# Optimization experiments

Measured on AMD Instinct MI355X. Metric: run time of the kernel, lower is better.

## Reference

```python
import jax, jax.numpy as jnp
import numpy as np

NNZ = 3355443          # int(4096*4096*(1-0.8))
IN_FEATURES = 4096
OUT_FEATURES = 4096
BATCH = 64
ACTIVE_THRESHOLD = 0.01


def setup_inputs() -> dict:
    key = jax.random.key(0)
    k1, k2, k3, k4 = jax.random.split(key, 4)
    x = jax.random.uniform(k1, (BATCH, IN_FEATURES), dtype=jnp.float32)
    row_indices = jax.random.randint(k2, (NNZ,), 0, OUT_FEATURES, dtype=jnp.int32)
    col_indices = jax.random.randint(k3, (NNZ,), 0, IN_FEATURES, dtype=jnp.int32)
    values = jax.random.normal(k4, (NNZ,), dtype=jnp.float32)
    bias = jnp.zeros((OUT_FEATURES,), dtype=jnp.float32)
    return {"x": x, "row_indices": row_indices, "col_indices": col_indices,
            "values": values, "bias": bias}


def reference(x, row_indices, col_indices, values, bias):
    # Event-driven gating: only columns with x > threshold contribute.
    # Equivalent to masking x, then a standard COO spmv per batch row.
    xm = jnp.where(x > ACTIVE_THRESHOLD, x, jnp.zeros((), x.dtype))   # [B, in]
    contrib = values[None, :] * xm[:, col_indices]                    # [B, nnz]
    out = jnp.zeros((x.shape[0], bias.shape[0]), dtype=x.dtype)
    out = out.at[:, row_indices].add(contrib)                         # scatter-add over rows
    return out + bias[None, :]
```

## Files before the change

kernel.cpp:

```cpp
#include <hip/hip_runtime.h>
#include <hip/hip_bf16.h>
#include <stdint.h>

#define IN_F 4096
#define OUT_F 4096
#define NBIN 512
#define SBLOCKS 410
#define REC_PER_SB 8192
#define SMAX 7424u
#define THRESH 0.01f

typedef unsigned int u32;
typedef unsigned short u16;
typedef __attribute__((ext_vector_type(8))) short short8;
typedef __attribute__((ext_vector_type(4))) float f32x4;

static constexpr size_t pad256(size_t x) { return (x + 255u) & ~(size_t)255u; }
static constexpr size_t WS_XB   = 0;
static constexpr size_t WS_CUR  = pad256(WS_XB + (size_t)512 * 64 * 8 * 2);
static constexpr size_t WS_BINS = pad256(WS_CUR + (size_t)NBIN * 4);
static constexpr size_t WS_PART = pad256(WS_BINS + (size_t)NBIN * SMAX * 4);
static constexpr size_t WS_NEEDED = WS_PART + (size_t)NBIN * 4096 * 4;

static __device__ __forceinline__ u16 f2bf(float v) {
  __hip_bfloat16 h = __float2bfloat16(v);
  return *reinterpret_cast<u16*>(&h);
}

__global__ __launch_bounds__(512) void k_init(u32* __restrict__ cur) {
  cur[threadIdx.x] = 0u;
}

__global__ __launch_bounds__(1024) void k_scatter(const int* __restrict__ rows,
                                                  const int* __restrict__ cols,
                                                  const float* __restrict__ vals, u32 nnz,
                                                  const float* __restrict__ x,
                                                  u16* __restrict__ xB,
                                                  u32* __restrict__ gcursor,
                                                  u32* __restrict__ sortb) {
  __shared__ u32 cnt[NBIN];
  __shared__ u32 pref[NBIN + 1];
  __shared__ u32 gbase[NBIN];
  __shared__ u32 srt[REC_PER_SB];
  __shared__ u16 srtb[REC_PER_SB];
  const int tid = threadIdx.x;
  const int lane = tid & 63;
  const int wid = tid >> 6;

  if (blockIdx.x < 32) {
    const int g = blockIdx.x * 1024 + tid;
    const int b = g & 63;
    const int kg = g >> 6;
    const float* src = x + (size_t)b * IN_F + kg * 8;
    const f32x4 a0 = *reinterpret_cast<const f32x4*>(src);
    const f32x4 a1 = *reinterpret_cast<const f32x4*>(src + 4);
    short8 o;
#pragma unroll
    for (int e = 0; e < 4; ++e) { float v = a0[e]; o[e] = (short)f2bf(v > THRESH ? v : 0.f); }
#pragma unroll
    for (int e = 0; e < 4; ++e) { float v = a1[e]; o[4 + e] = (short)f2bf(v > THRESH ? v : 0.f); }
    *reinterpret_cast<short8*>(xB + ((size_t)kg * 64 + b) * 8) = o;
  }

  if (tid < NBIN) cnt[tid] = 0;
  __syncthreads();
  const u32 base_i = blockIdx.x * (u32)REC_PER_SB;
  u32 rec[8], bkt[8], rk[8];
#pragma unroll
  for (int j = 0; j < 8; ++j) {
    const u32 i = base_i + (u32)j * 1024u + tid;
    bkt[j] = 0xffffffffu;
    if (i < nnz) {
      const u32 r = (u32)rows[i] & 4095u;
      const u32 c = (u32)cols[i] & 4095u;
      rec[j] = ((c & 511u) << 22) | ((r & 63u) << 16) | (u32)f2bf(vals[i]);
      bkt[j] = ((r >> 6) << 3) | (c >> 9);
      rk[j] = atomicAdd(&cnt[bkt[j]], 1u);
    }
  }
  __syncthreads();
  if (wid == 0) {
    u32 a[8]; u32 s = 0;
#pragma unroll
    for (int j = 0; j < 8; ++j) { a[j] = cnt[lane * 8 + j]; s += a[j]; }
    u32 xx = s;
#pragma unroll
    for (int d = 1; d < 64; d <<= 1) {
      const u32 y = (u32)__shfl_up((int)xx, d, 64);
      if (lane >= d) xx += y;
    }
    u32 e = xx - s;
#pragma unroll
    for (int j = 0; j < 8; ++j) { pref[lane * 8 + j] = e; e += a[j]; }
    if (lane == 63) pref[NBIN] = e;
  }
  __syncthreads();
#pragma unroll
  for (int j = 0; j < 8; ++j)
    if (bkt[j] != 0xffffffffu) {
      const u32 pos = pref[bkt[j]] + rk[j];
      srt[pos] = rec[j];
      srtb[pos] = (u16)bkt[j];
    }
  if (tid < NBIN) {
    const u32 len = pref[tid + 1] - pref[tid];
    gbase[tid] = len ? atomicAdd(&gcursor[tid], len) : 0u;
  }
  __syncthreads();
  const u32 tot = pref[NBIN];
#pragma unroll
  for (int j = 0; j < 8; ++j) {
    const u32 i = (u32)j * 1024u + tid;
    if (i < tot) {
      const u32 t = srtb[i];
      const u32 off = gbase[t] + (i - pref[t]);
      if (off < SMAX) sortb[(size_t)t * SMAX + off] = srt[i];
    }
  }
}

__global__ __launch_bounds__(1024, 4) void k_accum(const u32* __restrict__ sortb,
                                                   const u32* __restrict__ ntot,
                                                   const u16* __restrict__ xB,
                                                   float* __restrict__ part) {
  __shared__ float W[64 * 512];
  const u32 bin = blockIdx.x;
  const u32 ks = bin & 7;
  u32 n = ntot[bin];
  if (n > SMAX) n = SMAX;
  const u32* bb = sortb + (size_t)bin * SMAX;
  const int tid = threadIdx.x;
  const int lane = tid & 63;
  const int w = tid >> 6;
  const f32x4 zv = {0.f, 0.f, 0.f, 0.f};
#pragma unroll
  for (int j = 0; j < 8; ++j)
    *reinterpret_cast<f32x4*>(&W[j * 4096 + tid * 4]) = zv;
  __syncthreads();
#define ADDREC(RC) do {                                                     \
    const u32 rl_ = ((RC) >> 16) & 63u;                                     \
    const u32 cl_ = (((RC) >> 22) & 511u) ^ ((rl_ & 7u) << 2);              \
    unsafeAtomicAdd(&W[rl_ * 512u + cl_], __uint_as_float((RC) << 16));     \
  } while (0)
  u32 i = (u32)tid;
  for (; i + 3072u < n; i += 4096u) {
    const u32 r0 = bb[i], r1 = bb[i + 1024u], r2 = bb[i + 2048u], r3 = bb[i + 3072u];
    ADDREC(r0); ADDREC(r1); ADDREC(r2); ADDREC(r3);
  }
  for (; i < n; i += 1024u) { const u32 r0 = bb[i]; ADDREC(r0); }
#undef ADDREC
  __syncthreads();
  const int rt = w >> 2, bg = w & 3;
  const int fr = lane & 15;
  const int e8 = (lane >> 4) * 8;
  const int rl = rt * 16 + fr;
  const int xr = (rl & 7) << 2;
  f32x4 acc = zv;
  const u32 kbase = ks * 512u;
#pragma unroll
  for (int ck = 0; ck < 16; ++ck) {
    const int klb = ck * 32 + e8;
    const f32x4 wa = *reinterpret_cast<const f32x4*>(&W[rl * 512 + (klb ^ xr)]);
    const f32x4 wb = *reinterpret_cast<const f32x4*>(&W[rl * 512 + ((klb + 4) ^ xr)]);
    short8 af;
#pragma unroll
    for (int e = 0; e < 4; ++e) af[e] = (short)f2bf(wa[e]);
#pragma unroll
    for (int e = 0; e < 4; ++e) af[4 + e] = (short)f2bf(wb[e]);
    const u32 kabs = kbase + (u32)klb;
    const short8 bf = *reinterpret_cast<const short8*>(
        xB + ((size_t)(kabs >> 3) * 64 + (u32)(bg * 16 + fr)) * 8);
    acc = __builtin_amdgcn_mfma_f32_16x16x32_bf16(af, bf, acc, 0, 0, 0);
  }
  __syncthreads();
#pragma unroll
  for (int qq = 0; qq < 4; ++qq)
    W[(bg * 16 + fr) * 64 + rt * 16 + (lane >> 4) * 4 + qq] = acc[qq];
  __syncthreads();
  *reinterpret_cast<f32x4*>(&part[(size_t)bin * 4096 + tid * 4]) =
      *reinterpret_cast<const f32x4*>(&W[tid * 4]);
}

__global__ __launch_bounds__(1024) void k_combine(const float* __restrict__ part,
                                                  const float* __restrict__ bias,
                                                  float* __restrict__ out) {
  const u32 rg = blockIdx.x >> 2;
  const u32 idx = (blockIdx.x & 3) * 1024u + threadIdx.x;
  const u32 b = idx >> 6;
  const u32 r = idx & 63u;
  float sum = bias[rg * 64u + r];
  const float* p = part + (size_t)(rg * 8u) * 4096 + idx;
#pragma unroll
  for (int ks = 0; ks < 8; ++ks) sum += p[(size_t)ks * 4096];
  out[(size_t)b * OUT_F + rg * 64u + r] = sum;
}

__global__ __launch_bounds__(256) void k_bias_init(const float* __restrict__ bias,
                                                   float* __restrict__ out) {
  const int i = blockIdx.x * 256 + threadIdx.x;
  if (i < 64 * OUT_F) out[i] = bias[i & (OUT_F - 1)];
}

__global__ __launch_bounds__(256) void k_fallback(const int* __restrict__ rows,
                                                  const int* __restrict__ cols,
                                                  const float* __restrict__ vals,
                                                  const float* __restrict__ x,
                                                  float* __restrict__ out, int nnz) {
  const int gw = (int)(((u32)blockIdx.x * blockDim.x + threadIdx.x) >> 6);
  const int lane = threadIdx.x & 63;
  const int nw = (int)(((u32)gridDim.x * blockDim.x) >> 6);
  for (int i = gw; i < nnz; i += nw) {
    const int r = rows[i];
    const int c = cols[i];
    const float v = vals[i];
    const float xv = x[lane * IN_F + c];
    if (xv > THRESH) atomicAdd(&out[(size_t)lane * OUT_F + r], v * xv);
  }
}

extern "C" void kernel_launch(void* const* d_in, const int* in_sizes, int n_in,
                              void* d_out, int out_size, void* d_ws, size_t ws_size,
                              hipStream_t stream) {
  const float* x = (const float*)d_in[0];
  const int* rows = (const int*)d_in[1];
  const int* cols = (const int*)d_in[2];
  const float* vals = (const float*)d_in[3];
  const float* bias = (const float*)d_in[4];
  float* out = (float*)d_out;
  const int nnz = in_sizes[1];

  if (ws_size >= WS_NEEDED && nnz <= SBLOCKS * REC_PER_SB) {
    u16* xB = (u16*)((char*)d_ws + WS_XB);
    u32* cur = (u32*)((char*)d_ws + WS_CUR);
    u32* sortb = (u32*)((char*)d_ws + WS_BINS);
    float* part = (float*)((char*)d_ws + WS_PART);
    k_init<<<1, 512, 0, stream>>>(cur);
    k_scatter<<<SBLOCKS, 1024, 0, stream>>>(rows, cols, vals, (u32)nnz, x, xB, cur, sortb);
    k_accum<<<NBIN, 1024, 0, stream>>>(sortb, cur, xB, part);
    k_combine<<<256, 1024, 0, stream>>>(part, bias, out);
  } else {
    k_bias_init<<<(64 * OUT_F + 255) / 256, 256, 0, stream>>>(bias, out);
    k_fallback<<<4096, 256, 0, stream>>>(rows, cols, vals, x, out, nnz);
  }
}
```

Baseline: 60.13 us.

## Split accumulation into densify-to-bf16 pass and separate MFMA GEMM with fused bias

The fused accumulate-plus-MFMA kernel is split in two. One kernel densifies each bin's sparse records into a bf16 dense weight tile in global memory. A separate GEMM kernel then computes 16 output rows per block over the full K range, reducing across waves in shared memory and adding bias directly, which removes the fp32 partials buffer and the combine kernel. The cost is writing and re-reading a 32 MB bf16 dense weight matrix through global memory.

```diff
diff --git a/kernel.cpp b/kernel.cpp
--- a/kernel.cpp
+++ b/kernel.cpp
@@ -19,8 +19,8 @@
 static constexpr size_t WS_XB   = 0;
 static constexpr size_t WS_CUR  = pad256(WS_XB + (size_t)512 * 64 * 8 * 2);
 static constexpr size_t WS_BINS = pad256(WS_CUR + (size_t)NBIN * 4);
-static constexpr size_t WS_PART = pad256(WS_BINS + (size_t)NBIN * SMAX * 4);
-static constexpr size_t WS_NEEDED = WS_PART + (size_t)NBIN * 4096 * 4;
+static constexpr size_t WS_WD   = pad256(WS_BINS + (size_t)NBIN * SMAX * 4);
+static constexpr size_t WS_NEEDED = WS_WD + (size_t)NBIN * 64 * 512 * 2;
 
 static __device__ __forceinline__ u16 f2bf(float v) {
   __hip_bfloat16 h = __float2bfloat16(v);
@@ -119,19 +119,15 @@
   }
 }
 
-__global__ __launch_bounds__(1024, 4) void k_accum(const u32* __restrict__ sortb,
-                                                   const u32* __restrict__ ntot,
-                                                   const u16* __restrict__ xB,
-                                                   float* __restrict__ part) {
+__global__ __launch_bounds__(1024, 4) void k_densify(const u32* __restrict__ sortb,
+                                                     const u32* __restrict__ ntot,
+                                                     u16* __restrict__ wd) {
   __shared__ float W[64 * 512];
   const u32 bin = blockIdx.x;
-  const u32 ks = bin & 7;
   u32 n = ntot[bin];
   if (n > SMAX) n = SMAX;
   const u32* bb = sortb + (size_t)bin * SMAX;
   const int tid = threadIdx.x;
-  const int lane = tid & 63;
-  const int w = tid >> 6;
   const f32x4 zv = {0.f, 0.f, 0.f, 0.f};
 #pragma unroll
   for (int j = 0; j < 8; ++j)
@@ -150,49 +146,75 @@
   for (; i < n; i += 1024u) { const u32 r0 = bb[i]; ADDREC(r0); }
 #undef ADDREC
   __syncthreads();
-  const int rt = w >> 2, bg = w & 3;
-  const int fr = lane & 15;
+#pragma unroll
+  for (int j = 0; j < 4; ++j) {
+    const u32 idx = (u32)j * 8192u + (u32)tid * 8u;
+    const u32 rl = idx >> 9, cl = idx & 511u;
+    const u32 xr = (rl & 7u) << 2;
+    const f32x4 wa = *reinterpret_cast<const f32x4*>(&W[rl * 512u + (cl ^ xr)]);
+    const f32x4 wb = *reinterpret_cast<const f32x4*>(&W[rl * 512u + ((cl + 4u) ^ xr)]);
+    short8 o;
+#pragma unroll
+    for (int e = 0; e < 4; ++e) o[e] = (short)f2bf(wa[e]);
+#pragma unroll
+    for (int e = 0; e < 4; ++e) o[4 + e] = (short)f2bf(wb[e]);
+    *reinterpret_cast<short8*>(wd + (size_t)bin * 32768u + idx) = o;
+  }
+}
+
+__global__ __launch_bounds__(1024) void k_gemm(const u16* __restrict__ wd,
+                                               const u16* __restrict__ xB,
+                                               const float* __restrict__ bias,
+                                               float* __restrict__ out) {
+  __shared__ float R[16 * 1024];
+  const int tid = threadIdx.x;
+  const int lane = tid & 63;
+  const int w = tid >> 6;
+  const u32 t = blockIdx.x;
+  const int row = lane & 15;
   const int e8 = (lane >> 4) * 8;
-  const int rl = rt * 16 + fr;
-  const int xr = (rl & 7) << 2;
-  f32x4 acc = zv;
-  const u32 kbase = ks * 512u;
-#pragma unroll
-  for (int ck = 0; ck < 16; ++ck) {
-    const int klb = ck * 32 + e8;
-    const f32x4 wa = *reinterpret_cast<const f32x4*>(&W[rl * 512 + (klb ^ xr)]);
-    const f32x4 wb = *reinterpret_cast<const f32x4*>(&W[rl * 512 + ((klb + 4) ^ xr)]);
-    short8 af;
-#pragma unroll
-    for (int e = 0; e < 4; ++e) af[e] = (short)f2bf(wa[e]);
-#pragma unroll
-    for (int e = 0; e < 4; ++e) af[4 + e] = (short)f2bf(wb[e]);
-    const u32 kabs = kbase + (u32)klb;
-    const short8 bf = *reinterpret_cast<const short8*>(
-        xB + ((size_t)(kabs >> 3) * 64 + (u32)(bg * 16 + fr)) * 8);
-    acc = __builtin_amdgcn_mfma_f32_16x16x32_bf16(af, bf, acc, 0, 0, 0);
-  }
-  __syncthreads();
-#pragma unroll
-  for (int qq = 0; qq < 4; ++qq)
-    W[(bg * 16 + fr) * 64 + rt * 16 + (lane >> 4) * 4 + qq] = acc[qq];
-  __syncthreads();
-  *reinterpret_cast<f32x4*>(&part[(size_t)bin * 4096 + tid * 4]) =
-      *reinterpret_cast<const f32x4*>(&W[tid * 4]);
-}
-
-__global__ __launch_bounds__(1024) void k_combine(const float* __restrict__ part,
-                                                  const float* __restrict__ bias,
-                                                  float* __restrict__ out) {
-  const u32 rg = blockIdx.x >> 2;
-  const u32 idx = (blockIdx.x & 3) * 1024u + threadIdx.x;
-  const u32 b = idx >> 6;
-  const u32 r = idx & 63u;
-  float sum = bias[rg * 64u + r];
-  const float* p = part + (size_t)(rg * 8u) * 4096 + idx;
-#pragma unroll
-  for (int ks = 0; ks < 8; ++ks) sum += p[(size_t)ks * 4096];
-  out[(size_t)b * OUT_F + rg * 64u + r] = sum;
+
+  const f32x4 zv = {0.f, 0.f, 0.f, 0.f};
+  f32x4 acc0 = zv, acc1 = zv, acc2 = zv, acc3 = zv;
+  const u32 r = t * 16u + (u32)row;
+  const u32 rg = r >> 6;
+  const size_t abase = (size_t)(r & 63u) * 512u;
+#pragma unroll
+  for (int s = 0; s < 8; ++s) {
+    const int kabs = w * 256 + s * 32 + e8;
+    const u32 bin = rg * 8u + ((u32)kabs >> 9);
+    const short8 af = *reinterpret_cast<const short8*>(
+        wd + (size_t)bin * 32768u + abase + (u32)(kabs & 511));
+    const u16* bp = xB + (size_t)(kabs >> 3) * 512 + (u32)row * 8;
+    const short8 b0 = *reinterpret_cast<const short8*>(bp);
+    const short8 b1 = *reinterpret_cast<const short8*>(bp + 128);
+    const short8 b2 = *reinterpret_cast<const short8*>(bp + 256);
+    const short8 b3 = *reinterpret_cast<const short8*>(bp + 384);
+    acc0 = __builtin_amdgcn_mfma_f32_16x16x32_bf16(af, b0, acc0, 0, 0, 0);
+    acc1 = __builtin_amdgcn_mfma_f32_16x16x32_bf16(af, b1, acc1, 0, 0, 0);
+    acc2 = __builtin_amdgcn_mfma_f32_16x16x32_bf16(af, b2, acc2, 0, 0, 0);
+    acc3 = __builtin_amdgcn_mfma_f32_16x16x32_bf16(af, b3, acc3, 0, 0, 0);
+  }
+  {
+    const int ccol = lane & 15;
+    const int rb = (lane >> 4) * 4;
+#pragma unroll
+    for (int qq = 0; qq < 4; ++qq) R[((w * 4 + 0) * 16 + rb + qq) * 16 + ccol] = acc0[qq];
+#pragma unroll
+    for (int qq = 0; qq < 4; ++qq) R[((w * 4 + 1) * 16 + rb + qq) * 16 + ccol] = acc1[qq];
+#pragma unroll
+    for (int qq = 0; qq < 4; ++qq) R[((w * 4 + 2) * 16 + rb + qq) * 16 + ccol] = acc2[qq];
+#pragma unroll
+    for (int qq = 0; qq < 4; ++qq) R[((w * 4 + 3) * 16 + rb + qq) * 16 + ccol] = acc3[qq];
+  }
+  __syncthreads();
+  const int rl = tid & 15;
+  const int b = tid >> 4;
+  float sum = bias[t * 16u + rl];
+#pragma unroll
+  for (int w2 = 0; w2 < 16; ++w2)
+    sum += R[((w2 * 4 + (b >> 4)) * 16 + rl) * 16 + (b & 15)];
+  out[(size_t)b * OUT_F + t * 16u + rl] = sum;
 }
 
 __global__ __launch_bounds__(256) void k_bias_init(const float* __restrict__ bias,
@@ -233,11 +255,11 @@
     u16* xB = (u16*)((char*)d_ws + WS_XB);
     u32* cur = (u32*)((char*)d_ws + WS_CUR);
     u32* sortb = (u32*)((char*)d_ws + WS_BINS);
-    float* part = (float*)((char*)d_ws + WS_PART);
+    u16* wd = (u16*)((char*)d_ws + WS_WD);
     k_init<<<1, 512, 0, stream>>>(cur);
     k_scatter<<<SBLOCKS, 1024, 0, stream>>>(rows, cols, vals, (u32)nnz, x, xB, cur, sortb);
-    k_accum<<<NBIN, 1024, 0, stream>>>(sortb, cur, xB, part);
-    k_combine<<<256, 1024, 0, stream>>>(part, bias, out);
+    k_densify<<<NBIN, 1024, 0, stream>>>(sortb, cur, wd);
+    k_gemm<<<OUT_F / 16, 1024, 0, stream>>>(wd, xB, bias, out);
   } else {
     k_bias_init<<<(64 * OUT_F + 255) / 256, 256, 0, stream>>>(bias, out);
     k_fallback<<<4096, 256, 0, stream>>>(rows, cols, vals, x, out, nnz);
```

Measured after the change: 65.31 us. 1.09x slower.
